# Kernel tuning notes

Hardware: AMD Instinct MI355X
Metric: run time of the kernel (lower is better)

The kernel has to match this reference:

```python
import jax, jax.numpy as jnp
import numpy as np

B, T, C = 8, 4096, 1024
NH = 64          # module sets self.n_head = dim_head = 64
HD = C // NH     # 16


def setup_inputs() -> dict:
    key = jax.random.key(0)
    ks = jax.random.split(key, 9)
    s = 1.0 / np.sqrt(C).astype(np.float32)
    x = jax.random.normal(ks[0], (B, T, C), jnp.float32)
    Wq = jax.random.normal(ks[1], (C, C), jnp.float32) * s
    bq = jax.random.normal(ks[2], (C,), jnp.float32) * 0.01
    Wk = jax.random.normal(ks[3], (C, C), jnp.float32) * s
    bk = jax.random.normal(ks[4], (C,), jnp.float32) * 0.01
    Wv = jax.random.normal(ks[5], (C, C), jnp.float32) * s
    bv = jax.random.normal(ks[6], (C,), jnp.float32) * 0.01
    Wp = jax.random.normal(ks[7], (C, C), jnp.float32) * s
    bp = jax.random.normal(ks[8], (C,), jnp.float32) * 0.01
    return {"x": x, "Wq": Wq, "bq": bq, "Wk": Wk, "bk": bk,
            "Wv": Wv, "bv": bv, "Wp": Wp, "bp": bp}


def _heads(t):
    # [B, T, C] -> [B, NH, T, HD]
    return t.reshape(B, T, NH, HD).transpose(0, 2, 1, 3)


def reference(x, Wq, bq, Wk, bk, Wv, bv, Wp, bp):
    # self-attention path: y = x; kv_mask=None (masked path is unreachable in source)
    q = _heads(x @ Wq.T + bq)
    k = _heads(x @ Wk.T + bk)
    v = _heads(x @ Wv.T + bv)
    q = jax.nn.softmax(q, axis=-1)
    k = jax.nn.softmax(k, axis=-1)
    k_cumsum = k.sum(axis=2, keepdims=True)               # [B, NH, 1, HD]
    D_inv = 1.0 / (q * k_cumsum).sum(axis=-1, keepdims=True)  # [B, NH, T, 1]
    context = jnp.einsum('bhtd,bhte->bhde', k, v)          # [B, NH, HD, HD]
    y = jnp.einsum('bhtd,bhde->bhte', q, context) * D_inv  # [B, NH, T, HD]
    y = y.transpose(0, 2, 1, 3).reshape(B, T, C)           # b h n d -> b n (h d)
    return y @ Wp.T + bp
```

## Files before the change

### kernel.cpp

```cpp
#include <hip/hip_runtime.h>
#include <stdint.h>


typedef __attribute__((ext_vector_type(8))) __bf16 bf16x8;
typedef __attribute__((ext_vector_type(4))) float f32x4;
typedef __attribute__((ext_vector_type(4))) unsigned int u32x4;
typedef __attribute__((ext_vector_type(4))) unsigned short u16x4;

#define AS1 __attribute__((address_space(1)))
#define AS3 __attribute__((address_space(3)))

__device__ __forceinline__ unsigned short f2bf(float f) {
  unsigned int u = __builtin_bit_cast(unsigned int, f);
  u += 0x7FFFu + ((u >> 16) & 1u);
  return (unsigned short)(u >> 16);
}

__device__ __forceinline__ void gl_lds16(const unsigned short* g, unsigned short* l) {
  __builtin_amdgcn_global_load_lds((const AS1 unsigned int*)g, (AS3 unsigned int*)l, 16, 0, 0);
}

__global__ __launch_bounds__(256)
void cvt_all(const float* __restrict__ x,
             const float* __restrict__ w0, const float* __restrict__ w1,
             const float* __restrict__ w2, const float* __restrict__ w3,
             unsigned short* __restrict__ xb, unsigned short* __restrict__ wb) {
  const int blk = blockIdx.x;
  if (blk < 2048) {
    int i = blk * 256 + threadIdx.x;
    #pragma unroll 4
    for (; i < 8388608; i += 524288) {
      f32x4 v = *(const f32x4*)(x + (size_t)i * 4);
      u16x4 o;
      o.x = f2bf(v.x); o.y = f2bf(v.y); o.z = f2bf(v.z); o.w = f2bf(v.w);
      *(u16x4*)(xb + (size_t)i * 4) = o;
    }
  } else {
    const int g = (blk - 2048) * 256 + threadIdx.x;
    const int w = g >> 17;
    const int r = g & 131071;
    const int f = r >> 6;
    const int l = r & 63;
    const int n = (f >> 5) * 16 + (l & 15);
    const int k = (f & 31) * 32 + (l >> 4) * 8;
    const float* ws[4] = {w0, w1, w2, w3};
    const float* src = ws[w] + (size_t)n * 1024 + k;
    f32x4 v0 = *(const f32x4*)src;
    f32x4 v1 = *(const f32x4*)(src + 4);
    u16x4 a, b;
    a.x = f2bf(v0.x); a.y = f2bf(v0.y); a.z = f2bf(v0.z); a.w = f2bf(v0.w);
    b.x = f2bf(v1.x); b.y = f2bf(v1.y); b.z = f2bf(v1.z); b.w = f2bf(v1.w);
    unsigned short* o = wb + (size_t)g * 8;
    *(u16x4*)o = a;
    *(u16x4*)(o + 4) = b;
  }
}

template<int KIND>
__global__ __launch_bounds__(256, 3)
void gemm_pipe(const unsigned short* __restrict__ A,
               const unsigned short* __restrict__ Wf,
               const float* __restrict__ b0, const float* __restrict__ b1,
               const float* __restrict__ b2,
               unsigned short* __restrict__ oq, unsigned short* __restrict__ okT,
               unsigned short* __restrict__ ovT, float* __restrict__ of)
{
  __shared__ __align__(16) unsigned short lds[24576];

  const int tid  = threadIdx.x;
  const int lane = tid & 63;
  const int wid  = tid >> 6;

  const int flat  = blockIdx.x;
  const int xcd   = flat & 7;
  const int i     = flat >> 3;
  const int bcg   = i >> 8;
  const int r     = i & 255;
  const int panel = r >> 3;
  const int c     = r & 7;
  const int brow  = (xcd * 32 + panel) * 128;
  const int bcol  = (bcg * 8 + c) * 128;

  const int srow = wid * 16 + (lane >> 2);
  const int scol = ((lane & 3) ^ ((lane >> 3) & 3)) << 3;
  const unsigned short* a_src = A + (size_t)(brow + srow) * 1024 + scol;
  unsigned short* Ldst = lds + wid * 512;

  const int wm = (wid >> 1) * 64;
  const int wn = (wid & 1) * 64;
  const int fr = lane & 15;
  const int fg = lane >> 4;
  const int aoff = (wm + fr) * 32 + ((fg ^ ((fr >> 1) & 3)) << 3);

  const unsigned short* wfp = Wf + ((size_t)((bcol + wn) >> 4) * 32) * 512 + lane * 8;

  const f32x4 fz = {0.f, 0.f, 0.f, 0.f};
  f32x4 acc[4][4];
  #pragma unroll
  for (int mt = 0; mt < 4; ++mt)
    #pragma unroll
    for (int nt = 0; nt < 4; ++nt) acc[mt][nt] = fz;

  auto stage = [&](int T, int sb) {
    unsigned short* d = Ldst + sb * 8192;
    const unsigned short* g = a_src + T * 64;
    gl_lds16(g,              d);
    gl_lds16(g + 65536,      d + 2048);
    gl_lds16(g + 32,         d + 4096);
    gl_lds16(g + 65536 + 32, d + 6144);
  };
  auto loadB = [&](int k32, bf16x8 (&dst)[4]) {
    #pragma unroll
    for (int nt = 0; nt < 4; ++nt)
      dst[nt] = __builtin_bit_cast(bf16x8,
        *(const u32x4*)(wfp + (size_t)k32 * 512 + (size_t)nt * 16384));
  };

  bf16x8 bEven[4], bOdd[4];

  stage(0, 0); stage(1, 1);
  loadB(0, bEven);
  asm volatile("s_waitcnt vmcnt(8)" ::: "memory");
  __builtin_amdgcn_sched_barrier(0);
  __builtin_amdgcn_s_barrier();

  for (int T = 0; T < 16; ++T) {
    loadB(2 * T + 1, bOdd);
    const unsigned short* Lb = lds + (T % 3) * 8192;
    bf16x8 af[8];
    #pragma unroll
    for (int mt = 0; mt < 4; ++mt) {
      af[mt]     = __builtin_bit_cast(bf16x8, *(const u32x4*)&Lb[aoff + mt * 512]);
      af[4 + mt] = __builtin_bit_cast(bf16x8, *(const u32x4*)&Lb[4096 + aoff + mt * 512]);
    }
    asm volatile("s_waitcnt vmcnt(4)" ::: "memory");
    __builtin_amdgcn_sched_barrier(0);
    if (T < 15) __builtin_amdgcn_s_barrier();
    if (T + 2 < 16) stage(T + 2, (T + 2) % 3);

    __builtin_amdgcn_s_setprio(1);
    #pragma unroll
    for (int mt = 0; mt < 4; ++mt)
      #pragma unroll
      for (int nt = 0; nt < 4; ++nt)
        acc[mt][nt] = __builtin_amdgcn_mfma_f32_16x16x32_bf16(af[mt], bEven[nt], acc[mt][nt], 0, 0, 0);
    __builtin_amdgcn_s_setprio(0);

    if (T < 15) loadB(2 * T + 2, bEven);

    __builtin_amdgcn_s_setprio(1);
    #pragma unroll
    for (int mt = 0; mt < 4; ++mt)
      #pragma unroll
      for (int nt = 0; nt < 4; ++nt)
        acc[mt][nt] = __builtin_amdgcn_mfma_f32_16x16x32_bf16(af[4 + mt], bOdd[nt], acc[mt][nt], 0, 0, 0);
    __builtin_amdgcn_s_setprio(0);
  }

  const int sec = (KIND == 0) ? (bcol >> 10) : 0;
  const float* bias = (KIND == 1) ? b0 : (sec == 0 ? b0 : (sec == 1 ? b1 : b2));

  #pragma unroll
  for (int nt = 0; nt < 4; ++nt) {
    const int n_glob = bcol + wn + nt * 16 + fr;
    const int nn = (KIND == 0) ? (n_glob & 1023) : n_glob;
    const float bv = bias[nn];
    #pragma unroll
    for (int mt = 0; mt < 4; ++mt) {
      const int m0 = brow + wm + mt * 16 + fg * 4;
      float vals[4];
      #pragma unroll
      for (int r2 = 0; r2 < 4; ++r2) vals[r2] = acc[mt][nt][r2] + bv;

      if (KIND == 0 && sec <= 1) {
        #pragma unroll
        for (int r2 = 0; r2 < 4; ++r2) {
          float e = __expf(vals[r2]);
          float sm = e;
          #pragma unroll
          for (int s = 1; s < 16; s <<= 1) sm += __shfl_xor(sm, s, 64);
          vals[r2] = e * __builtin_amdgcn_rcpf(sm);
        }
      }

      if (KIND == 1) {
        #pragma unroll
        for (int r2 = 0; r2 < 4; ++r2)
          of[(size_t)(m0 + r2) * 1024 + n_glob] = vals[r2];
      } else if (sec == 0) {
        #pragma unroll
        for (int r2 = 0; r2 < 4; ++r2)
          oq[(size_t)(m0 + r2) * 1024 + nn] = f2bf(vals[r2]);
      } else {
        unsigned short* o = (sec == 1) ? okT : ovT;
        const int bb = m0 >> 12;
        const int t0 = m0 & 4095;
        const int hh = nn >> 4;
        const int dd = nn & 15;
        u16x4 pk;
        pk.x = f2bf(vals[0]); pk.y = f2bf(vals[1]);
        pk.z = f2bf(vals[2]); pk.w = f2bf(vals[3]);
        *(u16x4*)&o[(((size_t)bb * 64 + hh) * 16 + dd) * 4096 + t0] = pk;
      }
    }
  }
}

__global__ __launch_bounds__(256)
void attn_kernel(const unsigned short* __restrict__ qb,
                 const unsigned short* __restrict__ kT,
                 const unsigned short* __restrict__ vT,
                 unsigned short* __restrict__ yb)
{
  const int pair = blockIdx.x;
  const int b    = pair >> 5;
  const int hp   = pair & 31;
  const int tid  = threadIdx.x;
  const int lane = tid & 63;
  const int wid  = tid >> 6;
  const int fr   = lane & 15;
  const int fg   = lane >> 4;

  const unsigned short* kT0 = kT + ((size_t)(b * 64 + hp * 2) * 16) * 4096;
  const unsigned short* vT0 = vT + ((size_t)(b * 64 + hp * 2) * 16) * 4096;
  const unsigned short* kT1 = kT0 + 16 * 4096;
  const unsigned short* vT1 = vT0 + 16 * 4096;

  const u32x4 uz = {0u, 0u, 0u, 0u};
  const f32x4 fz = {0.f, 0.f, 0.f, 0.f};
  const u32x4 uo = {0x3F803F80u, 0x3F803F80u, 0x3F803F80u, 0x3F803F80u};
  const bf16x8 ones = __builtin_bit_cast(bf16x8, uo);

  f32x4 cctx0 = fz, ckc0 = fz, cctx1 = fz, ckc1 = fz;
  #pragma unroll 2
  for (int t0 = wid * 1024; t0 < (wid + 1) * 1024; t0 += 32) {
    const size_t off = (size_t)fr * 4096 + t0 + fg * 8;
    bf16x8 ak0 = __builtin_bit_cast(bf16x8, *(const u32x4*)&kT0[off]);
    bf16x8 bv0 = __builtin_bit_cast(bf16x8, *(const u32x4*)&vT0[off]);
    bf16x8 ak1 = __builtin_bit_cast(bf16x8, *(const u32x4*)&kT1[off]);
    bf16x8 bv1 = __builtin_bit_cast(bf16x8, *(const u32x4*)&vT1[off]);
    cctx0 = __builtin_amdgcn_mfma_f32_16x16x32_bf16(ak0, bv0, cctx0, 0, 0, 0);
    ckc0  = __builtin_amdgcn_mfma_f32_16x16x32_bf16(ak0, ones, ckc0, 0, 0, 0);
    cctx1 = __builtin_amdgcn_mfma_f32_16x16x32_bf16(ak1, bv1, cctx1, 0, 0, 0);
    ckc1  = __builtin_amdgcn_mfma_f32_16x16x32_bf16(ak1, ones, ckc1, 0, 0, 0);
  }

  __shared__ float red[4][2][16][16];
  __shared__ float kcr[4][2][16];
  __shared__ float ctxf[2][16][16];
  __shared__ float kcf[2][16];

  #pragma unroll
  for (int r = 0; r < 4; ++r) {
    red[wid][0][fg * 4 + r][fr] = cctx0[r];
    red[wid][1][fg * 4 + r][fr] = cctx1[r];
  }
  if (fr == 0) {
    #pragma unroll
    for (int r = 0; r < 4; ++r) {
      kcr[wid][0][fg * 4 + r] = ckc0[r];
      kcr[wid][1][fg * 4 + r] = ckc1[r];
    }
  }
  __syncthreads();
  {
    const int d = (tid >> 4) & 15, e = tid & 15;
    #pragma unroll
    for (int hh = 0; hh < 2; ++hh)
      ctxf[hh][d][e] = red[0][hh][d][e] + red[1][hh][d][e] + red[2][hh][d][e] + red[3][hh][d][e];
    if (tid < 32) {
      const int hh = tid >> 4, dd = tid & 15;
      kcf[hh][dd] = kcr[0][hh][dd] + kcr[1][hh][dd] + kcr[2][hh][dd] + kcr[3][hh][dd];
    }
  }
  __syncthreads();

  bf16x8 bctx0 = __builtin_bit_cast(bf16x8, uz);
  bf16x8 bctx1 = __builtin_bit_cast(bf16x8, uz);
  bf16x8 bkc0  = __builtin_bit_cast(bf16x8, uz);
  bf16x8 bkc1  = __builtin_bit_cast(bf16x8, uz);
  if (fg < 2) {
    #pragma unroll
    for (int j = 0; j < 8; ++j) {
      const int d = fg * 8 + j;
      bctx0[j] = (__bf16)ctxf[0][d][fr];
      bkc0[j]  = (__bf16)kcf[0][d];
    }
  } else {
    #pragma unroll
    for (int j = 0; j < 8; ++j) {
      const int d = (fg - 2) * 8 + j;
      bctx1[j] = (__bf16)ctxf[1][d][fr];
      bkc1[j]  = (__bf16)kcf[1][d];
    }
  }

  const size_t cbase = (size_t)b * 4096 * 1024 + (size_t)hp * 32;

  for (int step = 0; step < 64; ++step) {
    const int t0 = step * 64 + wid * 16;
    bf16x8 af = __builtin_bit_cast(bf16x8,
        *(const u32x4*)&qb[cbase + (size_t)(t0 + fr) * 1024 + fg * 8]);
    f32x4 cy0 = __builtin_amdgcn_mfma_f32_16x16x32_bf16(af, bctx0, fz, 0, 0, 0);
    f32x4 cy1 = __builtin_amdgcn_mfma_f32_16x16x32_bf16(af, bctx1, fz, 0, 0, 0);
    f32x4 cd0 = __builtin_amdgcn_mfma_f32_16x16x32_bf16(af, bkc0,  fz, 0, 0, 0);
    f32x4 cd1 = __builtin_amdgcn_mfma_f32_16x16x32_bf16(af, bkc1,  fz, 0, 0, 0);
    #pragma unroll
    for (int r = 0; r < 4; ++r) {
      const int t = t0 + fg * 4 + r;
      const size_t o = cbase + (size_t)t * 1024;
      yb[o + fr]      = f2bf(cy0[r] * __builtin_amdgcn_rcpf(cd0[r]));
      yb[o + 16 + fr] = f2bf(cy1[r] * __builtin_amdgcn_rcpf(cd1[r]));
    }
  }
}

extern "C" void kernel_launch(void* const* d_in, const int* in_sizes, int n_in,
                              void* d_out, int out_size, void* d_ws, size_t ws_size,
                              hipStream_t stream)
{
  (void)in_sizes; (void)n_in; (void)out_size; (void)ws_size;
  const float* x  = (const float*)d_in[0];
  const float* Wq = (const float*)d_in[1];
  const float* bq = (const float*)d_in[2];
  const float* Wk = (const float*)d_in[3];
  const float* bk = (const float*)d_in[4];
  const float* Wv = (const float*)d_in[5];
  const float* bv = (const float*)d_in[6];
  const float* Wp = (const float*)d_in[7];
  const float* bp = (const float*)d_in[8];

  char* ws = (char*)d_ws;
  unsigned short* xb  = (unsigned short*)(ws);
  unsigned short* wb  = (unsigned short*)(ws + 67108864);
  unsigned short* qb  = (unsigned short*)(ws + 75497472);
  unsigned short* kTb = (unsigned short*)(ws + 142606336);
  unsigned short* vTb = (unsigned short*)(ws + 209715200);

  cvt_all<<<4096, 256, 0, stream>>>(x, Wq, Wk, Wv, Wp, xb, wb);

  gemm_pipe<0><<<6144, 256, 0, stream>>>(xb, wb, bq, bk, bv, qb, kTb, vTb, nullptr);

  attn_kernel<<<256, 256, 0, stream>>>(qb, kTb, vTb, xb );

  gemm_pipe<1><<<2048, 256, 0, stream>>>(xb , wb + 3145728, bp, bp, bp,
                                         nullptr, nullptr, nullptr, (float*)d_out);
}
```

Measured before the change: 456.1 us.

## Pre-swizzle x into MFMA fragment layout and drop LDS staging in QKV GEMM

The conversion kernel now writes x in bf16 in the same fragment-major layout as the weights, so the QKV GEMM loads A fragments straight from global memory into registers with a double-buffered register pipeline instead of staging through LDS with barriers. The projection GEMM becomes its own kernel that keeps LDS staging, with reordered waits and explicit vmcnt/lgkmcnt accounting. This removes LDS traffic and block barriers from the large GEMM. The cost is that each wave re-reads A from global or L2 without sharing, and the register prefetch depth is only one step.

```diff
diff --git a/kernel.cpp b/kernel.cpp
--- a/kernel.cpp
+++ b/kernel.cpp
@@ -24,19 +24,28 @@
 void cvt_all(const float* __restrict__ x,
              const float* __restrict__ w0, const float* __restrict__ w1,
              const float* __restrict__ w2, const float* __restrict__ w3,
-             unsigned short* __restrict__ xb, unsigned short* __restrict__ wb) {
+             unsigned short* __restrict__ xaf, unsigned short* __restrict__ wb) {
   const int blk = blockIdx.x;
-  if (blk < 2048) {
-    int i = blk * 256 + threadIdx.x;
+  if (blk < 4096) {
+    int g = blk * 256 + threadIdx.x;
     #pragma unroll 4
-    for (; i < 8388608; i += 524288) {
-      f32x4 v = *(const f32x4*)(x + (size_t)i * 4);
-      u16x4 o;
-      o.x = f2bf(v.x); o.y = f2bf(v.y); o.z = f2bf(v.z); o.w = f2bf(v.w);
-      *(u16x4*)(xb + (size_t)i * 4) = o;
+    for (int it = 0; it < 4; ++it, g += 1048576) {
+      const int f = g >> 6;
+      const int l = g & 63;
+      const int row = (f >> 5) * 16 + (l & 15);
+      const int k   = (f & 31) * 32 + (l >> 4) * 8;
+      const float* src = x + (size_t)row * 1024 + k;
+      f32x4 v0 = *(const f32x4*)src;
+      f32x4 v1 = *(const f32x4*)(src + 4);
+      u16x4 a, b;
+      a.x = f2bf(v0.x); a.y = f2bf(v0.y); a.z = f2bf(v0.z); a.w = f2bf(v0.w);
+      b.x = f2bf(v1.x); b.y = f2bf(v1.y); b.z = f2bf(v1.z); b.w = f2bf(v1.w);
+      unsigned short* o = xaf + (size_t)g * 8;
+      *(u16x4*)o = a;
+      *(u16x4*)(o + 4) = b;
     }
   } else {
-    const int g = (blk - 2048) * 256 + threadIdx.x;
+    const int g = (blk - 4096) * 256 + threadIdx.x;
     const int w = g >> 17;
     const int r = g & 131071;
     const int f = r >> 6;
@@ -56,17 +65,14 @@
   }
 }
 
-template<int KIND>
 __global__ __launch_bounds__(256, 3)
-void gemm_pipe(const unsigned short* __restrict__ A,
-               const unsigned short* __restrict__ Wf,
-               const float* __restrict__ b0, const float* __restrict__ b1,
-               const float* __restrict__ b2,
-               unsigned short* __restrict__ oq, unsigned short* __restrict__ okT,
-               unsigned short* __restrict__ ovT, float* __restrict__ of)
+void gemm_qkv(const unsigned short* __restrict__ Af,
+              const unsigned short* __restrict__ Wf,
+              const float* __restrict__ b0, const float* __restrict__ b1,
+              const float* __restrict__ b2,
+              unsigned short* __restrict__ oq, unsigned short* __restrict__ okT,
+              unsigned short* __restrict__ ovT)
 {
-  __shared__ __align__(16) unsigned short lds[24576];
-
   const int tid  = threadIdx.x;
   const int lane = tid & 63;
   const int wid  = tid >> 6;
@@ -81,18 +87,26 @@
   const int brow  = (xcd * 32 + panel) * 128;
   const int bcol  = (bcg * 8 + c) * 128;
 
-  const int srow = wid * 16 + (lane >> 2);
-  const int scol = ((lane & 3) ^ ((lane >> 3) & 3)) << 3;
-  const unsigned short* a_src = A + (size_t)(brow + srow) * 1024 + scol;
-  unsigned short* Ldst = lds + wid * 512;
-
   const int wm = (wid >> 1) * 64;
   const int wn = (wid & 1) * 64;
   const int fr = lane & 15;
   const int fg = lane >> 4;
-  const int aoff = (wm + fr) * 32 + ((fg ^ ((fr >> 1) & 3)) << 3);
-
+
+  const unsigned short* afp = Af + ((size_t)((brow + wm) >> 4) * 32) * 512 + lane * 8;
   const unsigned short* wfp = Wf + ((size_t)((bcol + wn) >> 4) * 32) * 512 + lane * 8;
+
+  auto loadA = [&](int t, bf16x8 (&dst)[4]) {
+    #pragma unroll
+    for (int mt = 0; mt < 4; ++mt)
+      dst[mt] = __builtin_bit_cast(bf16x8,
+        *(const u32x4*)(afp + (size_t)t * 512 + (size_t)mt * 16384));
+  };
+  auto loadB = [&](int t, bf16x8 (&dst)[4]) {
+    #pragma unroll
+    for (int nt = 0; nt < 4; ++nt)
+      dst[nt] = __builtin_bit_cast(bf16x8,
+        *(const u32x4*)(wfp + (size_t)t * 512 + (size_t)nt * 16384));
+  };
 
   const f32x4 fz = {0.f, 0.f, 0.f, 0.f};
   f32x4 acc[4][4];
@@ -101,69 +115,37 @@
     #pragma unroll
     for (int nt = 0; nt < 4; ++nt) acc[mt][nt] = fz;
 
-  auto stage = [&](int T, int sb) {
-    unsigned short* d = Ldst + sb * 8192;
-    const unsigned short* g = a_src + T * 64;
-    gl_lds16(g,              d);
-    gl_lds16(g + 65536,      d + 2048);
-    gl_lds16(g + 32,         d + 4096);
-    gl_lds16(g + 65536 + 32, d + 6144);
-  };
-  auto loadB = [&](int k32, bf16x8 (&dst)[4]) {
-    #pragma unroll
-    for (int nt = 0; nt < 4; ++nt)
-      dst[nt] = __builtin_bit_cast(bf16x8,
-        *(const u32x4*)(wfp + (size_t)k32 * 512 + (size_t)nt * 16384));
-  };
-
-  bf16x8 bEven[4], bOdd[4];
-
-  stage(0, 0); stage(1, 1);
-  loadB(0, bEven);
-  asm volatile("s_waitcnt vmcnt(8)" ::: "memory");
-  __builtin_amdgcn_sched_barrier(0);
-  __builtin_amdgcn_s_barrier();
-
-  for (int T = 0; T < 16; ++T) {
-    loadB(2 * T + 1, bOdd);
-    const unsigned short* Lb = lds + (T % 3) * 8192;
-    bf16x8 af[8];
-    #pragma unroll
-    for (int mt = 0; mt < 4; ++mt) {
-      af[mt]     = __builtin_bit_cast(bf16x8, *(const u32x4*)&Lb[aoff + mt * 512]);
-      af[4 + mt] = __builtin_bit_cast(bf16x8, *(const u32x4*)&Lb[4096 + aoff + mt * 512]);
-    }
-    asm volatile("s_waitcnt vmcnt(4)" ::: "memory");
+  bf16x8 aC[4], aN[4], bC[4], bN[4];
+
+  loadA(0, aC); loadB(0, bC);
+
+  auto body = [&](int t, bf16x8 (&ac)[4], bf16x8 (&bc)[4],
+                  bf16x8 (&an)[4], bf16x8 (&bn)[4]) {
+    if (t + 1 < 32) { loadA(t + 1, an); loadB(t + 1, bn); }
+    if (t + 1 < 32) asm volatile("s_waitcnt vmcnt(8)" ::: "memory");
+    else            asm volatile("s_waitcnt vmcnt(0)" ::: "memory");
     __builtin_amdgcn_sched_barrier(0);
-    if (T < 15) __builtin_amdgcn_s_barrier();
-    if (T + 2 < 16) stage(T + 2, (T + 2) % 3);
-
     __builtin_amdgcn_s_setprio(1);
     #pragma unroll
     for (int mt = 0; mt < 4; ++mt)
       #pragma unroll
       for (int nt = 0; nt < 4; ++nt)
-        acc[mt][nt] = __builtin_amdgcn_mfma_f32_16x16x32_bf16(af[mt], bEven[nt], acc[mt][nt], 0, 0, 0);
+        acc[mt][nt] = __builtin_amdgcn_mfma_f32_16x16x32_bf16(ac[mt], bc[nt], acc[mt][nt], 0, 0, 0);
     __builtin_amdgcn_s_setprio(0);
-
-    if (T < 15) loadB(2 * T + 2, bEven);
-
-    __builtin_amdgcn_s_setprio(1);
-    #pragma unroll
-    for (int mt = 0; mt < 4; ++mt)
-      #pragma unroll
-      for (int nt = 0; nt < 4; ++nt)
-        acc[mt][nt] = __builtin_amdgcn_mfma_f32_16x16x32_bf16(af[4 + mt], bOdd[nt], acc[mt][nt], 0, 0, 0);
-    __builtin_amdgcn_s_setprio(0);
-  }
-
-  const int sec = (KIND == 0) ? (bcol >> 10) : 0;
-  const float* bias = (KIND == 1) ? b0 : (sec == 0 ? b0 : (sec == 1 ? b1 : b2));
+  };
+
+  for (int t = 0; t < 32; t += 2) {
+    body(t,     aC, bC, aN, bN);
+    body(t + 1, aN, bN, aC, bC);
+  }
+
+  const int sec = bcol >> 10;
+  const float* bias = (sec == 0 ? b0 : (sec == 1 ? b1 : b2));
 
   #pragma unroll
   for (int nt = 0; nt < 4; ++nt) {
     const int n_glob = bcol + wn + nt * 16 + fr;
-    const int nn = (KIND == 0) ? (n_glob & 1023) : n_glob;
+    const int nn = n_glob & 1023;
     const float bv = bias[nn];
     #pragma unroll
     for (int mt = 0; mt < 4; ++mt) {
@@ -172,7 +154,7 @@
       #pragma unroll
       for (int r2 = 0; r2 < 4; ++r2) vals[r2] = acc[mt][nt][r2] + bv;
 
-      if (KIND == 0 && sec <= 1) {
+      if (sec <= 1) {
         #pragma unroll
         for (int r2 = 0; r2 < 4; ++r2) {
           float e = __expf(vals[r2]);
@@ -183,11 +165,7 @@
         }
       }
 
-      if (KIND == 1) {
-        #pragma unroll
-        for (int r2 = 0; r2 < 4; ++r2)
-          of[(size_t)(m0 + r2) * 1024 + n_glob] = vals[r2];
-      } else if (sec == 0) {
+      if (sec == 0) {
         #pragma unroll
         for (int r2 = 0; r2 < 4; ++r2)
           oq[(size_t)(m0 + r2) * 1024 + nn] = f2bf(vals[r2]);
@@ -206,6 +184,126 @@
   }
 }
 
+__global__ __launch_bounds__(256, 3)
+void gemm_proj(const unsigned short* __restrict__ A,
+               const unsigned short* __restrict__ Wf,
+               const float* __restrict__ b0,
+               float* __restrict__ of)
+{
+  __shared__ __align__(16) unsigned short lds[24576];
+
+  const int tid  = threadIdx.x;
+  const int lane = tid & 63;
+  const int wid  = tid >> 6;
+
+  const int flat  = blockIdx.x;
+  const int xcd   = flat & 7;
+  const int i     = flat >> 3;
+  const int r     = i & 255;
+  const int panel = r >> 3;
+  const int c     = r & 7;
+  const int brow  = (xcd * 32 + panel) * 128;
+  const int bcol  = c * 128;
+
+  const int srow = wid * 16 + (lane >> 2);
+  const int scol = ((lane & 3) ^ ((lane >> 3) & 3)) << 3;
+  const unsigned short* a_src = A + (size_t)(brow + srow) * 1024 + scol;
+  unsigned short* Ldst = lds + wid * 512;
+
+  const int wm = (wid >> 1) * 64;
+  const int wn = (wid & 1) * 64;
+  const int fr = lane & 15;
+  const int fg = lane >> 4;
+  const int aoff = (wm + fr) * 32 + ((fg ^ ((fr >> 1) & 3)) << 3);
+
+  const unsigned short* wfp = Wf + ((size_t)((bcol + wn) >> 4) * 32) * 512 + lane * 8;
+
+  const f32x4 fz = {0.f, 0.f, 0.f, 0.f};
+  f32x4 acc[4][4];
+  #pragma unroll
+  for (int mt = 0; mt < 4; ++mt)
+    #pragma unroll
+    for (int nt = 0; nt < 4; ++nt) acc[mt][nt] = fz;
+
+  auto stage = [&](int T, int sb) {
+    unsigned short* d = Ldst + sb * 8192;
+    const unsigned short* g = a_src + T * 64;
+    gl_lds16(g,              d);
+    gl_lds16(g + 65536,      d + 2048);
+    gl_lds16(g + 32,         d + 4096);
+    gl_lds16(g + 65536 + 32, d + 6144);
+  };
+  auto loadB = [&](int k32, bf16x8 (&dst)[4]) {
+    #pragma unroll
+    for (int nt = 0; nt < 4; ++nt)
+      dst[nt] = __builtin_bit_cast(bf16x8,
+        *(const u32x4*)(wfp + (size_t)k32 * 512 + (size_t)nt * 16384));
+  };
+
+  bf16x8 bEven[4], bOdd[4];
+
+  stage(0, 0); stage(1, 1);
+  loadB(0, bEven);
+  asm volatile("s_waitcnt vmcnt(8)" ::: "memory");
+  __builtin_amdgcn_sched_barrier(0);
+  __builtin_amdgcn_s_barrier();
+
+  for (int T = 0; T < 16; ++T) {
+    const unsigned short* Lb = lds + (T % 3) * 8192;
+    bf16x8 af[8];
+    #pragma unroll
+    for (int mt = 0; mt < 4; ++mt) {
+      af[mt]     = __builtin_bit_cast(bf16x8, *(const u32x4*)&Lb[aoff + mt * 512]);
+      af[4 + mt] = __builtin_bit_cast(bf16x8, *(const u32x4*)&Lb[4096 + aoff + mt * 512]);
+    }
+    asm volatile("s_waitcnt lgkmcnt(0)" ::: "memory");
+    __builtin_amdgcn_sched_barrier(0);
+    if (T + 2 < 16) stage(T + 2, (T + 2) % 3);
+    loadB(2 * T + 1, bOdd);
+    if (T <= 13)      asm volatile("s_waitcnt vmcnt(8)" ::: "memory");
+    else              asm volatile("s_waitcnt vmcnt(4)" ::: "memory");
+    __builtin_amdgcn_sched_barrier(0);
+    if (T < 15) __builtin_amdgcn_s_barrier();
+
+    __builtin_amdgcn_s_setprio(1);
+    #pragma unroll
+    for (int mt = 0; mt < 4; ++mt)
+      #pragma unroll
+      for (int nt = 0; nt < 4; ++nt)
+        acc[mt][nt] = __builtin_amdgcn_mfma_f32_16x16x32_bf16(af[mt], bEven[nt], acc[mt][nt], 0, 0, 0);
+    __builtin_amdgcn_s_setprio(0);
+
+    if (T <= 14) loadB(2 * T + 2, bEven);
+    if (T <= 13)      asm volatile("s_waitcnt vmcnt(8)" ::: "memory");
+    else if (T == 14) asm volatile("s_waitcnt vmcnt(4)" ::: "memory");
+    else              asm volatile("s_waitcnt vmcnt(0)" ::: "memory");
+    __builtin_amdgcn_sched_barrier(0);
+
+    __builtin_amdgcn_s_setprio(1);
+    #pragma unroll
+    for (int mt = 0; mt < 4; ++mt)
+      #pragma unroll
+      for (int nt = 0; nt < 4; ++nt)
+        acc[mt][nt] = __builtin_amdgcn_mfma_f32_16x16x32_bf16(af[4 + mt], bOdd[nt], acc[mt][nt], 0, 0, 0);
+    __builtin_amdgcn_s_setprio(0);
+  }
+
+  const float bv = b0[bcol + wn + 0];
+  (void)bv;
+  #pragma unroll
+  for (int nt = 0; nt < 4; ++nt) {
+    const int n_glob = bcol + wn + nt * 16 + fr;
+    const float bvn = b0[n_glob];
+    #pragma unroll
+    for (int mt = 0; mt < 4; ++mt) {
+      const int m0 = brow + wm + mt * 16 + fg * 4;
+      #pragma unroll
+      for (int r2 = 0; r2 < 4; ++r2)
+        of[(size_t)(m0 + r2) * 1024 + n_glob] = acc[mt][nt][r2] + bvn;
+    }
+  }
+}
+
 __global__ __launch_bounds__(256)
 void attn_kernel(const unsigned short* __restrict__ qb,
                  const unsigned short* __restrict__ kT,
@@ -331,18 +429,17 @@
   const float* bp = (const float*)d_in[8];
 
   char* ws = (char*)d_ws;
-  unsigned short* xb  = (unsigned short*)(ws);
+  unsigned short* xaf = (unsigned short*)(ws);
   unsigned short* wb  = (unsigned short*)(ws + 67108864);
   unsigned short* qb  = (unsigned short*)(ws + 75497472);
   unsigned short* kTb = (unsigned short*)(ws + 142606336);
   unsigned short* vTb = (unsigned short*)(ws + 209715200);
 
-  cvt_all<<<4096, 256, 0, stream>>>(x, Wq, Wk, Wv, Wp, xb, wb);
-
-  gemm_pipe<0><<<6144, 256, 0, stream>>>(xb, wb, bq, bk, bv, qb, kTb, vTb, nullptr);
-
-  attn_kernel<<<256, 256, 0, stream>>>(qb, kTb, vTb, xb );
-
-  gemm_pipe<1><<<2048, 256, 0, stream>>>(xb , wb + 3145728, bp, bp, bp,
-                                         nullptr, nullptr, nullptr, (float*)d_out);
-}
+  cvt_all<<<6144, 256, 0, stream>>>(x, Wq, Wk, Wv, Wp, xaf, wb);
+
+  gemm_qkv<<<6144, 256, 0, stream>>>(xaf, wb, bq, bk, bv, qb, kTb, vTb);
+
+  attn_kernel<<<256, 256, 0, stream>>>(qb, kTb, vTb, xaf );
+
+  gemm_proj<<<2048, 256, 0, stream>>>(xaf , wb + 3145728, bp, (float*)d_out);
+}
```

After: 466.5 us. +2.3%, slower.
